# Performance work log

Hardware: AMD Instinct MI355X
Metric: run time of the kernel (lower is better)

Reference implementation:

```python
import jax, jax.numpy as jnp
from jax import lax
import numpy as np

HIDDEN = 40
NUM_LAYERS = 7
B, H, W = 16, 64, 64
KS = 7
PAD = KS // 2  # 3

# mask for conv_2d type 'A': zero rows below center, zero right-of-center in
# the center row, and zero the center tap itself
_m = np.ones((1, 1, KS, KS), np.float32)
_m[:, :, PAD + 1:, :] = 0
_m[:, :, PAD, PAD + 1:] = 0
_m[:, :, PAD, PAD] = 0
MASK_A = jnp.asarray(_m)


def conv2d(x, w, pad):
    return lax.conv_general_dilated(x, w, (1, 1), pad,
                                    dimension_numbers=('NCHW', 'OIHW', 'NCHW'))


def setup_inputs() -> dict:
    key = jax.random.key(0)
    ks = jax.random.split(key, 12)
    s = 0.05
    return {
        'input_tensor': jax.random.normal(ks[0], (B, 1, H, W), jnp.float32),
        'target_tensor': jax.random.normal(ks[1], (B, 1, H, W), jnp.float32),
        # masked conv_2d(7,1,80) applied to target
        'w_is': jax.random.normal(ks[2], (2 * HIDDEN, 1, KS, KS), jnp.float32) * s,
        'b_is': jnp.ones((2 * HIDDEN,), jnp.float32),
        # conv_i_s: Conv2d(1, 80, 7, pad 3)
        'w_cis': jax.random.normal(ks[3], (2 * HIDDEN, 1, KS, KS), jnp.float32) * s,
        'b_cis': jax.random.normal(ks[4], (2 * HIDDEN,), jnp.float32) * s,
        # row convs: Conv2d(40, 40, [1,3], pad [0,1])
        'w_rh': jax.random.normal(ks[5], (HIDDEN, HIDDEN, 1, 3), jnp.float32) * s,
        'b_rh': jax.random.normal(ks[6], (HIDDEN,), jnp.float32) * s,
        'w_rc': jax.random.normal(ks[7], (HIDDEN, HIDDEN, 1, 3), jnp.float32) * s,
        'b_rc': jax.random.normal(ks[8], (HIDDEN,), jnp.float32) * s,
        # per-layer cell 1x1 convs: 40 -> 160, stacked over layers
        'w_cell': jax.random.normal(ks[9], (NUM_LAYERS, 4 * HIDDEN, HIDDEN), jnp.float32) * s,
        'b_cell': jax.random.normal(ks[10], (NUM_LAYERS, 4 * HIDDEN), jnp.float32) * s,
        # conv_out: Conv2d(40, 256, 1)
        'w_out': jax.random.normal(ks[11], (256, HIDDEN), jnp.float32) * s,
        'b_out': jnp.zeros((256,), jnp.float32),
    }


def reference(input_tensor, target_tensor, w_is, b_is, w_cis, b_cis,
              w_rh, b_rh, w_rc, b_rc, w_cell, b_cell, w_out, b_out):
    same7 = ((PAD, PAD), (PAD, PAD))
    # i_s = cat([conv_i_s(input), masked_conv(target)], dim=1) -> [B, 160, H, W]
    i_s_input = conv2d(input_tensor, w_cis, same7) + b_cis[None, :, None, None]
    i_s_target = conv2d(target_tensor, w_is * MASK_A, same7) + b_is[None, :, None, None]
    i_s = jnp.concatenate([i_s_input, i_s_target], axis=1)

    h0 = jnp.zeros((B, HIDDEN, 1, W), i_s.dtype)
    c0 = jnp.zeros((B, HIDDEN, 1, W), i_s.dtype)

    def step(carry, x_t):  # x_t: [B, 160, 1, W]
        h, c = carry
        h = conv2d(h, w_rh, ((0, 0), (1, 1))) + b_rh[None, :, None, None]
        c = conv2d(c, w_rc, ((0, 0), (1, 1))) + b_rc[None, :, None, None]
        for l in range(NUM_LAYERS):
            h_conv = jnp.einsum('oc,bcrw->borw', w_cell[l], h) + b_cell[l][None, :, None, None]
            combined = x_t + h_conv
            cc_i, cc_f, cc_o, cc_g = jnp.split(combined, 4, axis=1)
            i = jax.nn.sigmoid(cc_i)
            f = jax.nn.sigmoid(cc_f)
            o = jax.nn.sigmoid(cc_o)
            g = jnp.tanh(cc_g)
            c = f * c + i * g
            h = o * jnp.tanh(c)
        return (h, c), h

    xs = jnp.moveaxis(i_s, 2, 0)[:, :, :, None, :]  # [H, B, 160, 1, W]
    _, hs = lax.scan(step, (h0, c0), xs)            # hs: [H, B, 40, 1, W]
    hidden = jnp.moveaxis(hs[:, :, :, 0, :], 0, 2)  # [B, 40, H, W]
    out = jnp.einsum('oc,bchw->bohw', w_out, hidden) + b_out[None, :, None, None]
    return jax.nn.relu(out)
```

## Files before the change

### kernel.cpp

```cpp
#include <hip/hip_runtime.h>


typedef __bf16 bf16x8 __attribute__((ext_vector_type(8)));
typedef __bf16 bf16x4 __attribute__((ext_vector_type(4)));
typedef float  f32x4  __attribute__((ext_vector_type(4)));

#define SC1 (-1.44269504089f)
#define SC2 (-2.88539008178f)

#define STP 56
#define HLS 896
#define CWS 17

#define BARRIER_LGKM() __asm__ volatile("s_waitcnt lgkmcnt(0)\ns_barrier" ::: "memory")

__global__ __launch_bounds__(512) void convprep_kernel(
        const float* __restrict__ inp, const float* __restrict__ tgt,
        const float* __restrict__ w_is, const float* __restrict__ b_is,
        const float* __restrict__ w_cis, const float* __restrict__ b_cis,
        const float* __restrict__ wcell, const float* __restrict__ wrh,
        const float* __restrict__ wrc, const float* __restrict__ bcell,
        const float* __restrict__ brh, const float* __restrict__ brc,
        const float* __restrict__ w_out, const float* __restrict__ b_out,
        float* __restrict__ x_ws, __bf16* __restrict__ wsA) {
    const int bidx = blockIdx.x;
    const int tid = threadIdx.x;
    if (bidx >= 640) {
        int i = (bidx - 640) * 512 + tid;
        if (i >= 137216) return;
        float val = 0.0f;
        if (i < 35840) {
            int j = i & 7, lane = (i >> 3) & 63, lm = i >> 9;
            int mt = lm % 10, l = lm / 10;
            int k = (lane >> 4) * 8 + j, m = lane & 15, r = m & 3;
            int row = r * 40 + 4 * mt + (m >> 2);
            val = wcell[(l * 160 + row) * 40 + k] * (r == 3 ? SC2 : SC1);
        } else if (i < 71680) {
            int i2 = i - 35840;
            int j = i2 & 7, lane = (i2 >> 3) & 63, lm = i2 >> 9;
            int mt = lm % 10, l = lm / 10;
            int k = 32 + (lane >> 4) * 8 + j, m = lane & 15, r = m & 3;
            int row = r * 40 + 4 * mt + (m >> 2);
            float s = (r == 3 ? SC2 : SC1);
            if (k < 40)       val = wcell[(l * 160 + row) * 40 + k] * s;
            else if (k == 40) val = bcell[l * 160 + row] * s;
        } else if (i < 80896) {
            int i3 = i - 71680;
            int j = i3 & 7, lane = (i3 >> 3) & 63, idx = i3 >> 9;
            int mtc = idx % 3, t2 = idx / 3, dx = t2 % 3, cv = t2 / 3;
            int k = (lane >> 4) * 8 + j;
            int ch = 16 * mtc + (lane & 15);
            const float* w = cv ? wrc : wrh;
            if (ch < 40) val = w[(ch * 40 + k) * 3 + dx];
        } else if (i < 90112) {
            int i4 = i - 80896;
            int j = i4 & 7, lane = (i4 >> 3) & 63, idx = i4 >> 9;
            int mtc = idx % 3, t2 = idx / 3, dx = t2 % 3, cv = t2 / 3;
            int k = 32 + (lane >> 4) * 8 + j;
            int ch = 16 * mtc + (lane & 15);
            if (ch < 40) {
                const float* w = cv ? wrc : wrh;
                if (k < 40)                    val = w[(ch * 40 + k) * 3 + dx];
                else if (k == 40 && dx == 1)   val = (cv ? brc : brh)[ch];
            }
        } else if (i < 105472) {
            int i5 = i - 90112;
            int j = i5 & 7, lane = (i5 >> 3) & 63, idx = i5 >> 9;
            int mt = idx % 10, dx = idx / 10;
            int k = (lane >> 4) * 8 + j, m = lane & 15, r = m & 3;
            int row = r * 40 + 4 * mt + (m >> 2);
            float s = (r == 3 ? SC2 : SC1);
            float acc = 0.0f;
            for (int mm = 0; mm < 40; mm++)
                acc = __builtin_fmaf(wcell[row * 40 + mm],
                                     wrh[(mm * 40 + k) * 3 + dx], acc);
            val = acc * s;
        } else if (i < 120832) {
            int i6 = i - 105472;
            int j = i6 & 7, lane = (i6 >> 3) & 63, idx = i6 >> 9;
            int mt = idx % 10, dx = idx / 10;
            int k = 32 + (lane >> 4) * 8 + j, m = lane & 15, r = m & 3;
            int row = r * 40 + 4 * mt + (m >> 2);
            float s = (r == 3 ? SC2 : SC1);
            if (k < 40) {
                float acc = 0.0f;
                for (int mm = 0; mm < 40; mm++)
                    acc = __builtin_fmaf(wcell[row * 40 + mm],
                                         wrh[(mm * 40 + k) * 3 + dx], acc);
                val = acc * s;
            } else if (k == 40 && dx == 1) {
                float acc = bcell[row];
                for (int mm = 0; mm < 40; mm++)
                    acc = __builtin_fmaf(wcell[row * 40 + mm], brh[mm], acc);
                val = acc * s;
            }
        } else if (i < 129024) {
            int i7 = i - 120832;
            int j = i7 & 7, lane = (i7 >> 3) & 63, ot = i7 >> 9;
            int k = (lane >> 4) * 8 + j;
            int o = ot * 16 + (lane & 15);
            val = w_out[o * 40 + k];
        } else {
            int i8 = i - 129024;
            int j = i8 & 7, lane = (i8 >> 3) & 63, ot = i8 >> 9;
            int k = 32 + (lane >> 4) * 8 + j;
            int o = ot * 16 + (lane & 15);
            if (k < 40)       val = w_out[o * 40 + k];
            else if (k == 40) val = b_out[o];
        }
        wsA[i] = (__bf16)val;
        return;
    }
    const int b = bidx / 40, cc = bidx - b * 40;
    const int wv = tid >> 6, x = tid & 63;
    const int y0 = wv * 8;
    const float* ib = inp + b * 4096;
    const float* tb = tgt + b * 4096;
    const float* w0 = w_cis + cc * 49;
    const float* w1 = w_cis + (40 + cc) * 49;
    const float* w2 = w_is + cc * 49;
    const float* w3 = w_is + (40 + cc) * 49;
    const float bias0 = b_cis[cc], bias1 = b_cis[40 + cc];
    const float bias2 = b_is[cc],  bias3 = b_is[40 + cc];
    const int g = x >> 4, l16 = x & 15;
    const int jj = cc >> 2, qq = cc & 3;

    float pin[7][7], ptg[4][7];
    auto ldrow = [&](const float* base, int yy, float* dst) {
#pragma unroll
        for (int dx = 0; dx < 7; dx++) {
            int xx = x + dx - 3;
            bool ok = (yy >= 0 && yy < 64 && xx >= 0 && xx < 64);
            dst[dx] = ok ? base[yy * 64 + xx] : 0.0f;
        }
    };
#pragma unroll
    for (int r = 0; r < 7; r++) ldrow(ib, y0 + r - 3, pin[r]);
#pragma unroll
    for (int r = 0; r < 4; r++) ldrow(tb, y0 + r - 3, ptg[r]);

#pragma unroll
    for (int iy = 0; iy < 8; iy++) {
        const int y = y0 + iy;
        if (iy > 0) {
#pragma unroll
            for (int r = 0; r < 6; r++)
#pragma unroll
                for (int dx = 0; dx < 7; dx++) pin[r][dx] = pin[r + 1][dx];
            ldrow(ib, y + 3, pin[6]);
#pragma unroll
            for (int r = 0; r < 3; r++)
#pragma unroll
                for (int dx = 0; dx < 7; dx++) ptg[r][dx] = ptg[r + 1][dx];
            ldrow(tb, y, ptg[3]);
        }
        float a0 = bias0, a1 = bias1, a2 = bias2, a3 = bias3;
#pragma unroll
        for (int dy = 0; dy < 7; dy++)
#pragma unroll
            for (int dx = 0; dx < 7; dx++) {
                a0 = __builtin_fmaf(w0[dy * 7 + dx], pin[dy][dx], a0);
                a1 = __builtin_fmaf(w1[dy * 7 + dx], pin[dy][dx], a1);
            }
#pragma unroll
        for (int dy = 0; dy < 3; dy++)
#pragma unroll
            for (int dx = 0; dx < 7; dx++) {
                a2 = __builtin_fmaf(w2[dy * 7 + dx], ptg[dy][dx], a2);
                a3 = __builtin_fmaf(w3[dy * 7 + dx], ptg[dy][dx], a3);
            }
#pragma unroll
        for (int dx = 0; dx < 3; dx++) {
            a2 = __builtin_fmaf(w2[21 + dx], ptg[3][dx], a2);
            a3 = __builtin_fmaf(w3[21 + dx], ptg[3][dx], a3);
        }
        size_t idx = (size_t)((((b * 64 + y) * 4 + g) * 10 + jj) * 4 + qq) * 64
                     + l16 * 4;
        *(f32x4*)&x_ws[idx] = f32x4{a0 * SC1, a1 * SC1, a2 * SC1, a3 * SC2};
    }
}

__global__ __launch_bounds__(640, 1) void rnn_kernel(
        const float* __restrict__ x_ws, const __bf16* __restrict__ wsA,
        unsigned long long* __restrict__ halo_ws, float* __restrict__ out) {
    __shared__ __align__(16) __bf16 hC[18 * STP + 64];
    __shared__ __align__(16) __bf16 cC[18 * STP + 64];
    __shared__ __align__(16) __bf16 hL[2 * HLS + 32];
    __shared__ float cwf[40 * CWS];
    __shared__ unsigned cflag[4];

    const int bid = blockIdx.x, g = bid >> 4, b = bid & 15;
    const int tid = threadIdx.x, wv = tid >> 6, lane = tid & 63;
    const int q = lane >> 4, l16 = lane & 15, cc = 4 * wv + q;
    const int W0 = g * 16;

    for (int i = tid; i < 536; i += 640) {
        ((float*)hC)[i] = 0.0f;
        ((float*)cC)[i] = 0.0f;
    }
    for (int i = tid; i < 912; i += 640)
        ((float*)hL)[i] = 0.0f;
    for (int i = tid; i < 40 * CWS; i += 640) cwf[i] = 0.0f;
    if (tid < 4) cflag[tid] = 0xFFFFFFFFu;
    __syncthreads();
    if (tid < 18) { hC[tid * STP + 40] = (__bf16)1.0f; cC[tid * STP + 40] = (__bf16)1.0f; }
    if (tid < 32) hL[(tid >> 4) * HLS + (tid & 15) * STP + 40] = (__bf16)1.0f;
    __syncthreads();

    bf16x8 a0c[6], a1c[6];
#pragma unroll
    for (int l = 1; l < 7; l++) {
        a0c[l - 1] = *(const bf16x8*)&wsA[((l * 10 + wv) * 64 + lane) * 8];
        a1c[l - 1] = *(const bf16x8*)&wsA[35840 + ((l * 10 + wv) * 64 + lane) * 8];
    }
    bf16x8 f0c[3], f1c[3];
#pragma unroll
    for (int dx = 0; dx < 3; dx++) {
        f0c[dx] = *(const bf16x8*)&wsA[90112 + ((dx * 10 + wv) * 64 + lane) * 8];
        f1c[dx] = *(const bf16x8*)&wsA[105472 + ((dx * 10 + wv) * 64 + lane) * 8];
    }
    bf16x8 cva0[3], cva1[3];
    if (wv >= 3 && wv < 6) {
        int mtc = wv - 3;
#pragma unroll
        for (int dx = 0; dx < 3; dx++) {
            int it = (3 + dx) * 3 + mtc;
            cva0[dx] = *(const bf16x8*)&wsA[71680 + (it * 64 + lane) * 8];
            cva1[dx] = *(const bf16x8*)&wsA[80896 + (it * 64 + lane) * 8];
        }
    }
    int nt = 0, tb0 = 0;
    if (wv == 0)      { nt = 4; tb0 = 0; }
    else if (wv == 1) { nt = 3; tb0 = 3; }
    else if (wv == 2) { nt = 3; tb0 = 6; }
    else if (wv == 6) { nt = 3; tb0 = 9; }
    else if (wv == 7) { nt = 3; tb0 = 12; }
    bf16x8 o0c[4], o1c[4];
#pragma unroll
    for (int i = 0; i < 4; i++) {
        if (i < nt) {
            int ot = (i == 3) ? 15 : tb0 + i;
            o0c[i] = *(const bf16x8*)&wsA[120832 + (ot * 64 + lane) * 8];
            o1c[i] = *(const bf16x8*)&wsA[129024 + (ot * 64 + lane) * 8];
        }
    }

    float c_reg = 0.0f;
    const size_t xstride = 10240;
    const size_t xbase0 = (size_t)(b * 64) * xstride
        + (((size_t)g * 10 + wv) * 4 + q) * 64 + l16 * 4;
    f32x4 xv = *(const f32x4*)&x_ws[xbase0];

    for (int t = 0; t < 64; t++) {
        f32x4 xn = xv;
        if (t < 63) xn = *(const f32x4*)&x_ws[xbase0 + (size_t)(t + 1) * xstride];

        if (wv >= 3 && wv < 6) {
            f32x4 ac = f32x4{0.f, 0.f, 0.f, 0.f};
#pragma unroll
            for (int dx = 0; dx < 3; dx++) {
                bf16x8 b0 = *(const bf16x8*)&cC[(l16 + dx) * STP + q * 8];
                bf16x8 b1 = *(const bf16x8*)&cC[(l16 + dx) * STP + 32 + q * 8];
                ac = __builtin_amdgcn_mfma_f32_16x16x32_bf16(cva0[dx], b0, ac, 0, 0, 0);
                ac = __builtin_amdgcn_mfma_f32_16x16x32_bf16(cva1[dx], b1, ac, 0, 0, 0);
            }
            int mtc = wv - 3, ch0 = 16 * mtc + 4 * q;
            if (ch0 < 40) {
#pragma unroll
                for (int r = 0; r < 4; r++) cwf[(ch0 + r) * CWS + l16] = ac[r];
            }
            __asm__ volatile("s_waitcnt lgkmcnt(0)" ::: "memory");
            if (lane == 0)
                __hip_atomic_store(&cflag[mtc], (unsigned)t,
                                   __ATOMIC_RELAXED, __HIP_MEMORY_SCOPE_WORKGROUP);
        }

        f32x4 acc0 = f32x4{0.f, 0.f, 0.f, 0.f};
#pragma unroll
        for (int dx = 0; dx < 3; dx++) {
            bf16x8 b0 = *(const bf16x8*)&hC[(l16 + dx) * STP + q * 8];
            bf16x8 b1 = *(const bf16x8*)&hC[(l16 + dx) * STP + 32 + q * 8];
            acc0 = __builtin_amdgcn_mfma_f32_16x16x32_bf16(f0c[dx], b0, acc0, 0, 0, 0);
            acc0 = __builtin_amdgcn_mfma_f32_16x16x32_bf16(f1c[dx], b1, acc0, 0, 0, 0);
        }

        if (t > 0 && nt) {
            int y = t - 1;
            bf16x8 bo0 = *(const bf16x8*)&hC[(l16 + 1) * STP + q * 8];
            bf16x8 bo1 = *(const bf16x8*)&hC[(l16 + 1) * STP + 32 + q * 8];
#pragma unroll
            for (int i = 0; i < 4; i++) {
                if (i < nt) {
                    int ot = (i == 3) ? 15 : tb0 + i;
                    f32x4 oa = __builtin_amdgcn_mfma_f32_16x16x32_bf16(
                        o0c[i], bo0, f32x4{0.f, 0.f, 0.f, 0.f}, 0, 0, 0);
                    oa = __builtin_amdgcn_mfma_f32_16x16x32_bf16(o1c[i], bo1, oa, 0, 0, 0);
                    int o0 = ot * 16 + 4 * q;
#pragma unroll
                    for (int r = 0; r < 4; r++)
                        out[((size_t)(b * 256 + o0 + r) * 64 + y) * 64 + W0 + l16] =
                            fmaxf(oa[r], 0.0f);
                }
            }
        }

        {
            int jj = wv >> 2;
            while (__hip_atomic_load(&cflag[jj], __ATOMIC_RELAXED,
                                     __HIP_MEMORY_SCOPE_WORKGROUP) != (unsigned)t)
                __builtin_amdgcn_s_sleep(1);
            __asm__ volatile("" ::: "memory");
        }

#pragma unroll
        for (int l = 0; l < 7; l++) {
            f32x4 acc;
            if (l == 0) {
                acc = acc0;
                c_reg = cwf[cc * CWS + l16];
            } else {
                const __bf16* hb = &hL[(l & 1) * HLS];
                bf16x8 b0 = *(const bf16x8*)&hb[l16 * STP + q * 8];
                bf16x8 b1 = *(const bf16x8*)&hb[l16 * STP + 32 + q * 8];
                acc = __builtin_amdgcn_mfma_f32_16x16x32_bf16(
                    a0c[l - 1], b0, f32x4{0.f, 0.f, 0.f, 0.f}, 0, 0, 0);
                acc = __builtin_amdgcn_mfma_f32_16x16x32_bf16(a1c[l - 1], b1, acc, 0, 0, 0);
            }
            float Ei = __builtin_amdgcn_exp2f(fminf(acc[0] + xv[0], 44.f));
            float Ef = __builtin_amdgcn_exp2f(fminf(acc[1] + xv[1], 44.f));
            float Eo = __builtin_amdgcn_exp2f(fminf(acc[2] + xv[2], 44.f));
            float Eg = __builtin_amdgcn_exp2f(fminf(acc[3] + xv[3], 44.f));
            float f = __builtin_amdgcn_rcpf(1.0f + Ef);
            float ig = (1.0f - Eg) * __builtin_amdgcn_rcpf((1.0f + Ei) * (1.0f + Eg));
            float c = __builtin_fmaf(f, c_reg, ig);
            c_reg = c;
            float Ec = __builtin_amdgcn_exp2f(fminf(SC2 * c, 44.f));
            float h = (1.0f - Ec) * __builtin_amdgcn_rcpf((1.0f + Eo) * (1.0f + Ec));
            if (l < 6) {
                hL[((l + 1) & 1) * HLS + l16 * STP + cc] = (__bf16)h;
                BARRIER_LGKM();
            } else {
                hC[(l16 + 1) * STP + cc] = (__bf16)h;
                cC[(l16 + 1) * STP + cc] = (__bf16)c;
                if (t < 63) {
                    unsigned short h16 = __builtin_bit_cast(unsigned short, (__bf16)h);
                    unsigned short c16 = __builtin_bit_cast(unsigned short, (__bf16)c);
                    unsigned long long v = ((unsigned long long)(unsigned)t << 32)
                        | ((unsigned)c16 << 16) | (unsigned)h16;
                    if (l16 == 0 && g > 0)
                        __hip_atomic_store(
                            &halo_ws[((bid * 2 + 0) * 2 + (t & 1)) * 40 + cc], v,
                            __ATOMIC_RELAXED, __HIP_MEMORY_SCOPE_AGENT);
                    if (l16 == 15 && g < 3)
                        __hip_atomic_store(
                            &halo_ws[((bid * 2 + 1) * 2 + (t & 1)) * 40 + cc], v,
                            __ATOMIC_RELAXED, __HIP_MEMORY_SCOPE_AGENT);
                }
            }
        }

        if (t < 63) {
            if (wv == 8 && g > 0 && lane < 40) {
                const unsigned long long* src =
                    &halo_ws[(((bid - 16) * 2 + 1) * 2 + (t & 1)) * 40 + lane];
                unsigned long long v = __hip_atomic_load(
                    src, __ATOMIC_RELAXED, __HIP_MEMORY_SCOPE_AGENT);
                while ((unsigned)(v >> 32) != (unsigned)t) {
                    __builtin_amdgcn_s_sleep(1);
                    v = __hip_atomic_load(src, __ATOMIC_RELAXED,
                                          __HIP_MEMORY_SCOPE_AGENT);
                }
                hC[lane] = __builtin_bit_cast(__bf16, (unsigned short)(v & 0xffffu));
                cC[lane] = __builtin_bit_cast(__bf16, (unsigned short)((v >> 16) & 0xffffu));
            }
            if (wv == 9 && g < 3 && lane < 40) {
                const unsigned long long* src =
                    &halo_ws[(((bid + 16) * 2 + 0) * 2 + (t & 1)) * 40 + lane];
                unsigned long long v = __hip_atomic_load(
                    src, __ATOMIC_RELAXED, __HIP_MEMORY_SCOPE_AGENT);
                while ((unsigned)(v >> 32) != (unsigned)t) {
                    __builtin_amdgcn_s_sleep(1);
                    v = __hip_atomic_load(src, __ATOMIC_RELAXED,
                                          __HIP_MEMORY_SCOPE_AGENT);
                }
                hC[17 * STP + lane] = __builtin_bit_cast(__bf16, (unsigned short)(v & 0xffffu));
                cC[17 * STP + lane] = __builtin_bit_cast(__bf16, (unsigned short)((v >> 16) & 0xffffu));
            }
        }
        BARRIER_LGKM();
        xv = xn;
    }

    if (nt) {
        bf16x8 bo0 = *(const bf16x8*)&hC[(l16 + 1) * STP + q * 8];
        bf16x8 bo1 = *(const bf16x8*)&hC[(l16 + 1) * STP + 32 + q * 8];
#pragma unroll
        for (int i = 0; i < 4; i++) {
            if (i < nt) {
                int ot = (i == 3) ? 15 : tb0 + i;
                f32x4 oa = __builtin_amdgcn_mfma_f32_16x16x32_bf16(
                    o0c[i], bo0, f32x4{0.f, 0.f, 0.f, 0.f}, 0, 0, 0);
                oa = __builtin_amdgcn_mfma_f32_16x16x32_bf16(o1c[i], bo1, oa, 0, 0, 0);
                int o0 = ot * 16 + 4 * q;
#pragma unroll
                for (int r = 0; r < 4; r++)
                    out[((size_t)(b * 256 + o0 + r) * 64 + 63) * 64 + W0 + l16] =
                        fmaxf(oa[r], 0.0f);
            }
        }
    }
}

extern "C" void kernel_launch(void* const* d_in, const int* in_sizes, int n_in,
                              void* d_out, int out_size, void* d_ws,
                              size_t ws_size, hipStream_t stream) {
    const float* input  = (const float*)d_in[0];
    const float* target = (const float*)d_in[1];
    const float* w_is   = (const float*)d_in[2];
    const float* b_is   = (const float*)d_in[3];
    const float* w_cis  = (const float*)d_in[4];
    const float* b_cis  = (const float*)d_in[5];
    const float* w_rh   = (const float*)d_in[6];
    const float* b_rh   = (const float*)d_in[7];
    const float* w_rc   = (const float*)d_in[8];
    const float* b_rc   = (const float*)d_in[9];
    const float* w_cell = (const float*)d_in[10];
    const float* b_cell = (const float*)d_in[11];
    const float* w_out  = (const float*)d_in[12];
    const float* b_out  = (const float*)d_in[13];
    float* out = (float*)d_out;

    char* ws = (char*)d_ws;
    float*              x_ws    = (float*)ws;
    __bf16*             wsA     = (__bf16*)(ws + 41943040);
    unsigned long long* halo_ws = (unsigned long long*)(ws + 42217472);

    convprep_kernel<<<908, 512, 0, stream>>>(input, target, w_is, b_is,
                                             w_cis, b_cis, w_cell, w_rh,
                                             w_rc, b_cell, b_rh, b_rc,
                                             w_out, b_out, x_ws, wsA);
    rnn_kernel<<<64, 640, 0, stream>>>(x_ws, wsA, halo_ws, out);
}
```

Measured before the change: 395.4 us.

## Offload output projection to two dedicated extra waves in RNN kernel

The RNN block grows from 10 to 12 waves. The two new waves handle the 40->256 output projection and its global stores, and the 10 recurrence waves no longer carry that work on their critical path. The extra waves still join every per-layer barrier, so the hope is that the output MFMAs and stores overlap with the serial LSTM chain. The cost is more barrier participants per step and more register pressure: each output wave holds 8 weight tiles, and all waves declare the a/f arrays.

Result: slower. 689.1 us (+74.3%).

```diff
diff --git a/kernel.cpp b/kernel.cpp
--- a/kernel.cpp
+++ b/kernel.cpp
@@ -180,7 +180,7 @@
     }
 }
 
-__global__ __launch_bounds__(640, 1) void rnn_kernel(
+__global__ __launch_bounds__(768, 1) void rnn_kernel(
         const float* __restrict__ x_ws, const __bf16* __restrict__ wsA,
         unsigned long long* __restrict__ halo_ws, float* __restrict__ out) {
     __shared__ __align__(16) __bf16 hC[18 * STP + 64];
@@ -194,13 +194,13 @@
     const int q = lane >> 4, l16 = lane & 15, cc = 4 * wv + q;
     const int W0 = g * 16;
 
-    for (int i = tid; i < 536; i += 640) {
+    for (int i = tid; i < 536; i += 768) {
         ((float*)hC)[i] = 0.0f;
         ((float*)cC)[i] = 0.0f;
     }
-    for (int i = tid; i < 912; i += 640)
+    for (int i = tid; i < 912; i += 768)
         ((float*)hL)[i] = 0.0f;
-    for (int i = tid; i < 40 * CWS; i += 640) cwf[i] = 0.0f;
+    for (int i = tid; i < 40 * CWS; i += 768) cwf[i] = 0.0f;
     if (tid < 4) cflag[tid] = 0xFFFFFFFFu;
     __syncthreads();
     if (tid < 18) { hC[tid * STP + 40] = (__bf16)1.0f; cC[tid * STP + 40] = (__bf16)1.0f; }
@@ -208,16 +208,18 @@
     __syncthreads();
 
     bf16x8 a0c[6], a1c[6];
-#pragma unroll
-    for (int l = 1; l < 7; l++) {
-        a0c[l - 1] = *(const bf16x8*)&wsA[((l * 10 + wv) * 64 + lane) * 8];
-        a1c[l - 1] = *(const bf16x8*)&wsA[35840 + ((l * 10 + wv) * 64 + lane) * 8];
-    }
     bf16x8 f0c[3], f1c[3];
-#pragma unroll
-    for (int dx = 0; dx < 3; dx++) {
-        f0c[dx] = *(const bf16x8*)&wsA[90112 + ((dx * 10 + wv) * 64 + lane) * 8];
-        f1c[dx] = *(const bf16x8*)&wsA[105472 + ((dx * 10 + wv) * 64 + lane) * 8];
+    if (wv < 10) {
+#pragma unroll
+        for (int l = 1; l < 7; l++) {
+            a0c[l - 1] = *(const bf16x8*)&wsA[((l * 10 + wv) * 64 + lane) * 8];
+            a1c[l - 1] = *(const bf16x8*)&wsA[35840 + ((l * 10 + wv) * 64 + lane) * 8];
+        }
+#pragma unroll
+        for (int dx = 0; dx < 3; dx++) {
+            f0c[dx] = *(const bf16x8*)&wsA[90112 + ((dx * 10 + wv) * 64 + lane) * 8];
+            f1c[dx] = *(const bf16x8*)&wsA[105472 + ((dx * 10 + wv) * 64 + lane) * 8];
+        }
     }
     bf16x8 cva0[3], cva1[3];
     if (wv >= 3 && wv < 6) {
@@ -229,17 +231,11 @@
             cva1[dx] = *(const bf16x8*)&wsA[80896 + (it * 64 + lane) * 8];
         }
     }
-    int nt = 0, tb0 = 0;
-    if (wv == 0)      { nt = 4; tb0 = 0; }
-    else if (wv == 1) { nt = 3; tb0 = 3; }
-    else if (wv == 2) { nt = 3; tb0 = 6; }
-    else if (wv == 6) { nt = 3; tb0 = 9; }
-    else if (wv == 7) { nt = 3; tb0 = 12; }
-    bf16x8 o0c[4], o1c[4];
-#pragma unroll
-    for (int i = 0; i < 4; i++) {
-        if (i < nt) {
-            int ot = (i == 3) ? 15 : tb0 + i;
+    bf16x8 o0c[8], o1c[8];
+    if (wv >= 10) {
+#pragma unroll
+        for (int i = 0; i < 8; i++) {
+            int ot = (wv - 10) * 8 + i;
             o0c[i] = *(const bf16x8*)&wsA[120832 + (ot * 64 + lane) * 8];
             o1c[i] = *(const bf16x8*)&wsA[129024 + (ot * 64 + lane) * 8];
         }
@@ -248,12 +244,14 @@
     float c_reg = 0.0f;
     const size_t xstride = 10240;
     const size_t xbase0 = (size_t)(b * 64) * xstride
-        + (((size_t)g * 10 + wv) * 4 + q) * 64 + l16 * 4;
-    f32x4 xv = *(const f32x4*)&x_ws[xbase0];
+        + (((size_t)g * 10 + ((wv < 10) ? wv : 0)) * 4 + q) * 64 + l16 * 4;
+    f32x4 xv = f32x4{0.f, 0.f, 0.f, 0.f};
+    if (wv < 10) xv = *(const f32x4*)&x_ws[xbase0];
 
     for (int t = 0; t < 64; t++) {
         f32x4 xn = xv;
-        if (t < 63) xn = *(const f32x4*)&x_ws[xbase0 + (size_t)(t + 1) * xstride];
+        if (wv < 10 && t < 63)
+            xn = *(const f32x4*)&x_ws[xbase0 + (size_t)(t + 1) * xstride];
 
         if (wv >= 3 && wv < 6) {
             f32x4 ac = f32x4{0.f, 0.f, 0.f, 0.f};
@@ -275,36 +273,32 @@
                                    __ATOMIC_RELAXED, __HIP_MEMORY_SCOPE_WORKGROUP);
         }
 
-        f32x4 acc0 = f32x4{0.f, 0.f, 0.f, 0.f};
-#pragma unroll
-        for (int dx = 0; dx < 3; dx++) {
-            bf16x8 b0 = *(const bf16x8*)&hC[(l16 + dx) * STP + q * 8];
-            bf16x8 b1 = *(const bf16x8*)&hC[(l16 + dx) * STP + 32 + q * 8];
-            acc0 = __builtin_amdgcn_mfma_f32_16x16x32_bf16(f0c[dx], b0, acc0, 0, 0, 0);
-            acc0 = __builtin_amdgcn_mfma_f32_16x16x32_bf16(f1c[dx], b1, acc0, 0, 0, 0);
-        }
-
-        if (t > 0 && nt) {
+        if (wv >= 10 && t > 0) {
             int y = t - 1;
             bf16x8 bo0 = *(const bf16x8*)&hC[(l16 + 1) * STP + q * 8];
             bf16x8 bo1 = *(const bf16x8*)&hC[(l16 + 1) * STP + 32 + q * 8];
 #pragma unroll
-            for (int i = 0; i < 4; i++) {
-                if (i < nt) {
-                    int ot = (i == 3) ? 15 : tb0 + i;
-                    f32x4 oa = __builtin_amdgcn_mfma_f32_16x16x32_bf16(
-                        o0c[i], bo0, f32x4{0.f, 0.f, 0.f, 0.f}, 0, 0, 0);
-                    oa = __builtin_amdgcn_mfma_f32_16x16x32_bf16(o1c[i], bo1, oa, 0, 0, 0);
-                    int o0 = ot * 16 + 4 * q;
-#pragma unroll
-                    for (int r = 0; r < 4; r++)
-                        out[((size_t)(b * 256 + o0 + r) * 64 + y) * 64 + W0 + l16] =
-                            fmaxf(oa[r], 0.0f);
-                }
-            }
-        }
-
-        {
+            for (int i = 0; i < 8; i++) {
+                f32x4 oa = __builtin_amdgcn_mfma_f32_16x16x32_bf16(
+                    o0c[i], bo0, f32x4{0.f, 0.f, 0.f, 0.f}, 0, 0, 0);
+                oa = __builtin_amdgcn_mfma_f32_16x16x32_bf16(o1c[i], bo1, oa, 0, 0, 0);
+                int o0 = ((wv - 10) * 8 + i) * 16 + 4 * q;
+#pragma unroll
+                for (int r = 0; r < 4; r++)
+                    out[((size_t)(b * 256 + o0 + r) * 64 + y) * 64 + W0 + l16] =
+                        fmaxf(oa[r], 0.0f);
+            }
+        }
+
+        f32x4 acc0 = f32x4{0.f, 0.f, 0.f, 0.f};
+        if (wv < 10) {
+#pragma unroll
+            for (int dx = 0; dx < 3; dx++) {
+                bf16x8 b0 = *(const bf16x8*)&hC[(l16 + dx) * STP + q * 8];
+                bf16x8 b1 = *(const bf16x8*)&hC[(l16 + dx) * STP + 32 + q * 8];
+                acc0 = __builtin_amdgcn_mfma_f32_16x16x32_bf16(f0c[dx], b0, acc0, 0, 0, 0);
+                acc0 = __builtin_amdgcn_mfma_f32_16x16x32_bf16(f1c[dx], b1, acc0, 0, 0, 0);
+            }
             int jj = wv >> 2;
             while (__hip_atomic_load(&cflag[jj], __ATOMIC_RELAXED,
                                      __HIP_MEMORY_SCOPE_WORKGROUP) != (unsigned)t)
@@ -314,49 +308,51 @@
 
 #pragma unroll
         for (int l = 0; l < 7; l++) {
-            f32x4 acc;
-            if (l == 0) {
-                acc = acc0;
-                c_reg = cwf[cc * CWS + l16];
-            } else {
-                const __bf16* hb = &hL[(l & 1) * HLS];
-                bf16x8 b0 = *(const bf16x8*)&hb[l16 * STP + q * 8];
-                bf16x8 b1 = *(const bf16x8*)&hb[l16 * STP + 32 + q * 8];
-                acc = __builtin_amdgcn_mfma_f32_16x16x32_bf16(
-                    a0c[l - 1], b0, f32x4{0.f, 0.f, 0.f, 0.f}, 0, 0, 0);
-                acc = __builtin_amdgcn_mfma_f32_16x16x32_bf16(a1c[l - 1], b1, acc, 0, 0, 0);
-            }
-            float Ei = __builtin_amdgcn_exp2f(fminf(acc[0] + xv[0], 44.f));
-            float Ef = __builtin_amdgcn_exp2f(fminf(acc[1] + xv[1], 44.f));
-            float Eo = __builtin_amdgcn_exp2f(fminf(acc[2] + xv[2], 44.f));
-            float Eg = __builtin_amdgcn_exp2f(fminf(acc[3] + xv[3], 44.f));
-            float f = __builtin_amdgcn_rcpf(1.0f + Ef);
-            float ig = (1.0f - Eg) * __builtin_amdgcn_rcpf((1.0f + Ei) * (1.0f + Eg));
-            float c = __builtin_fmaf(f, c_reg, ig);
-            c_reg = c;
-            float Ec = __builtin_amdgcn_exp2f(fminf(SC2 * c, 44.f));
-            float h = (1.0f - Ec) * __builtin_amdgcn_rcpf((1.0f + Eo) * (1.0f + Ec));
-            if (l < 6) {
-                hL[((l + 1) & 1) * HLS + l16 * STP + cc] = (__bf16)h;
-                BARRIER_LGKM();
-            } else {
-                hC[(l16 + 1) * STP + cc] = (__bf16)h;
-                cC[(l16 + 1) * STP + cc] = (__bf16)c;
-                if (t < 63) {
-                    unsigned short h16 = __builtin_bit_cast(unsigned short, (__bf16)h);
-                    unsigned short c16 = __builtin_bit_cast(unsigned short, (__bf16)c);
-                    unsigned long long v = ((unsigned long long)(unsigned)t << 32)
-                        | ((unsigned)c16 << 16) | (unsigned)h16;
-                    if (l16 == 0 && g > 0)
-                        __hip_atomic_store(
-                            &halo_ws[((bid * 2 + 0) * 2 + (t & 1)) * 40 + cc], v,
-                            __ATOMIC_RELAXED, __HIP_MEMORY_SCOPE_AGENT);
-                    if (l16 == 15 && g < 3)
-                        __hip_atomic_store(
-                            &halo_ws[((bid * 2 + 1) * 2 + (t & 1)) * 40 + cc], v,
-                            __ATOMIC_RELAXED, __HIP_MEMORY_SCOPE_AGENT);
+            if (wv < 10) {
+                f32x4 acc;
+                if (l == 0) {
+                    acc = acc0;
+                    c_reg = cwf[cc * CWS + l16];
+                } else {
+                    const __bf16* hb = &hL[(l & 1) * HLS];
+                    bf16x8 b0 = *(const bf16x8*)&hb[l16 * STP + q * 8];
+                    bf16x8 b1 = *(const bf16x8*)&hb[l16 * STP + 32 + q * 8];
+                    acc = __builtin_amdgcn_mfma_f32_16x16x32_bf16(
+                        a0c[l - 1], b0, f32x4{0.f, 0.f, 0.f, 0.f}, 0, 0, 0);
+                    acc = __builtin_amdgcn_mfma_f32_16x16x32_bf16(a1c[l - 1], b1, acc, 0, 0, 0);
                 }
-            }
+                float Ei = __builtin_amdgcn_exp2f(fminf(acc[0] + xv[0], 44.f));
+                float Ef = __builtin_amdgcn_exp2f(fminf(acc[1] + xv[1], 44.f));
+                float Eo = __builtin_amdgcn_exp2f(fminf(acc[2] + xv[2], 44.f));
+                float Eg = __builtin_amdgcn_exp2f(fminf(acc[3] + xv[3], 44.f));
+                float f = __builtin_amdgcn_rcpf(1.0f + Ef);
+                float ig = (1.0f - Eg) * __builtin_amdgcn_rcpf((1.0f + Ei) * (1.0f + Eg));
+                float c = __builtin_fmaf(f, c_reg, ig);
+                c_reg = c;
+                float Ec = __builtin_amdgcn_exp2f(fminf(SC2 * c, 44.f));
+                float h = (1.0f - Ec) * __builtin_amdgcn_rcpf((1.0f + Eo) * (1.0f + Ec));
+                if (l < 6) {
+                    hL[((l + 1) & 1) * HLS + l16 * STP + cc] = (__bf16)h;
+                } else {
+                    hC[(l16 + 1) * STP + cc] = (__bf16)h;
+                    cC[(l16 + 1) * STP + cc] = (__bf16)c;
+                    if (t < 63) {
+                        unsigned short h16 = __builtin_bit_cast(unsigned short, (__bf16)h);
+                        unsigned short c16 = __builtin_bit_cast(unsigned short, (__bf16)c);
+                        unsigned long long v = ((unsigned long long)(unsigned)t << 32)
+                            | ((unsigned)c16 << 16) | (unsigned)h16;
+                        if (l16 == 0 && g > 0)
+                            __hip_atomic_store(
+                                &halo_ws[((bid * 2 + 0) * 2 + (t & 1)) * 40 + cc], v,
+                                __ATOMIC_RELAXED, __HIP_MEMORY_SCOPE_AGENT);
+                        if (l16 == 15 && g < 3)
+                            __hip_atomic_store(
+                                &halo_ws[((bid * 2 + 1) * 2 + (t & 1)) * 40 + cc], v,
+                                __ATOMIC_RELAXED, __HIP_MEMORY_SCOPE_AGENT);
+                    }
+                }
+            }
+            if (l < 6) BARRIER_LGKM();
         }
 
         if (t < 63) {
@@ -391,22 +387,19 @@
         xv = xn;
     }
 
-    if (nt) {
+    if (wv >= 10) {
         bf16x8 bo0 = *(const bf16x8*)&hC[(l16 + 1) * STP + q * 8];
         bf16x8 bo1 = *(const bf16x8*)&hC[(l16 + 1) * STP + 32 + q * 8];
 #pragma unroll
-        for (int i = 0; i < 4; i++) {
-            if (i < nt) {
-                int ot = (i == 3) ? 15 : tb0 + i;
-                f32x4 oa = __builtin_amdgcn_mfma_f32_16x16x32_bf16(
-                    o0c[i], bo0, f32x4{0.f, 0.f, 0.f, 0.f}, 0, 0, 0);
-                oa = __builtin_amdgcn_mfma_f32_16x16x32_bf16(o1c[i], bo1, oa, 0, 0, 0);
-                int o0 = ot * 16 + 4 * q;
-#pragma unroll
-                for (int r = 0; r < 4; r++)
-                    out[((size_t)(b * 256 + o0 + r) * 64 + 63) * 64 + W0 + l16] =
-                        fmaxf(oa[r], 0.0f);
-            }
+        for (int i = 0; i < 8; i++) {
+            f32x4 oa = __builtin_amdgcn_mfma_f32_16x16x32_bf16(
+                o0c[i], bo0, f32x4{0.f, 0.f, 0.f, 0.f}, 0, 0, 0);
+            oa = __builtin_amdgcn_mfma_f32_16x16x32_bf16(o1c[i], bo1, oa, 0, 0, 0);
+            int o0 = ((wv - 10) * 8 + i) * 16 + 4 * q;
+#pragma unroll
+            for (int r = 0; r < 4; r++)
+                out[((size_t)(b * 256 + o0 + r) * 64 + 63) * 64 + W0 + l16] =
+                    fmaxf(oa[r], 0.0f);
         }
     }
 }
@@ -439,5 +432,5 @@
                                              w_cis, b_cis, w_cell, w_rh,
                                              w_rc, b_cell, b_rh, b_rc,
                                              w_out, b_out, x_ws, wsA);
-    rnn_kernel<<<64, 640, 0, stream>>>(x_ws, wsA, halo_ws, out);
+    rnn_kernel<<<64, 768, 0, stream>>>(x_ws, wsA, halo_ws, out);
 }
```
